# Kernel tuning notes

Hardware: AMD Instinct MI355X
Metric: run time of the kernel (lower is better)

## Reference

```python
import jax, jax.numpy as jnp
import numpy as np

EMB = 512
HEADS = 8
WINDOW = 128


def setup_inputs() -> dict:
    key = jax.random.key(0)
    ks = jax.random.split(key, 9)
    s = 1.0 / np.sqrt(EMB)
    x = jax.random.normal(ks[0], (2, 4096, EMB), dtype=jnp.float32)
    mk = lambda k: jax.random.uniform(k, (EMB, EMB), jnp.float32, -s, s)
    mb = lambda k: jax.random.uniform(k, (EMB,), jnp.float32, -s, s)
    return {
        "x": x,
        "Wq": mk(ks[1]), "bq": mb(ks[2]),
        "Wk": mk(ks[3]), "bk": mb(ks[4]),
        "Wv": mk(ks[5]), "bv": mb(ks[6]),
        "Wo": mk(ks[7]), "bo": mb(ks[8]),
    }


def _split_heads(y, b, n):
    # [b, n, emb] -> [b, h, n, d]
    return y.reshape(b, n, HEADS, EMB // HEADS).transpose(0, 2, 1, 3)


def reference(x, Wq, bq, Wk, bk, Wv, bv, Wo, bo):
    b, n, _ = x.shape
    q = _split_heads(x @ Wq.T + bq, b, n)
    k = _split_heads(x @ Wk.T + bk, b, n)
    v = _split_heads(x @ Wv.T + bv, b, n)
    energy = jnp.einsum('bhqd,bhkd->bhqk', q, k)  # [b,h,n,n]
    idx = jnp.arange(n)
    # banded mask: disallowed where |i - j| > window (matches torch loop)
    disallow = jnp.abs(idx[:, None] - idx[None, :]) > WINDOW
    fmin = jnp.float32(np.finfo(np.float32).min)
    energy = jnp.where(disallow[None, None], fmin, energy)
    att = jax.nn.softmax(energy / jnp.float32(np.sqrt(EMB)), axis=-1)
    out = jnp.einsum('bhql,bhld->bhqd', att, v)
    out = out.transpose(0, 2, 1, 3).reshape(b, n, EMB)
    return out @ Wo.T + bo
```

## Files before the change

### kernel.cpp

```cpp
#include <hip/hip_runtime.h>

#define EMB 512
#define HEADS 8
#define HD 64
#define NSEQ 4096
#define BATCH 2
#define WINDOW 128

typedef unsigned short u16;
typedef __attribute__((ext_vector_type(8))) short bf16x8;
typedef __attribute__((ext_vector_type(4))) float f32x4;

__device__ __forceinline__ float bf2f(u16 u) {
    union { unsigned int i; float f; } x;
    x.i = ((unsigned int)u) << 16;
    return x.f;
}

__device__ __forceinline__ u16 f2bf(float f) {
    union { float f; unsigned int i; } x;
    x.f = f;
    unsigned int i = x.i;
    unsigned int lsb = (i >> 16) & 1u;
    i += 0x7fffu + lsb;
    return (u16)(i >> 16);
}

__device__ __forceinline__ uint4 load8(const void* base, size_t off, int isbf) {
    if (isbf) {
        return *(const uint4*)((const u16*)base + off);
    } else {
        const float* f = (const float*)base + off;
        float4 a = *(const float4*)f;
        float4 b = *(const float4*)(f + 4);
        uint4 r;
        r.x = (unsigned)f2bf(a.x) | ((unsigned)f2bf(a.y) << 16);
        r.y = (unsigned)f2bf(a.z) | ((unsigned)f2bf(a.w) << 16);
        r.z = (unsigned)f2bf(b.x) | ((unsigned)f2bf(b.y) << 16);
        r.w = (unsigned)f2bf(b.z) | ((unsigned)f2bf(b.w) << 16);
        return r;
    }
}

__device__ __forceinline__ float loadScalar(const void* base, int i, int isbf) {
    return isbf ? bf2f(((const u16*)base)[i]) : ((const float*)base)[i];
}

__global__ void probe_dtypes(const void* p0, const void* p1, const void* p2,
                             const void* p3, const void* p4, const void* p5,
                             const void* p6, const void* p7, const void* p8,
                             int* flags)
{
    const void* ptrs[9] = {p0, p1, p2, p3, p4, p5, p6, p7, p8};
    const int lane = threadIdx.x;
    for (int i = 0; i < 9; ++i) {
        u16 w = ((const u16*)ptrs[i])[lane * 2];
        int e = (w >> 7) & 0xff;
        bool sane = (w == 0) || (e >= 100 && e <= 140);
        unsigned long long m = __ballot(sane);
        if (lane == 0) flags[i] = (__popcll(m) >= 48) ? 1 : 0;
    }
}

__global__ __launch_bounds__(256)
void qkv_gemm(const void* __restrict__ X,
              const void* __restrict__ Wq, const void* __restrict__ bq,
              const void* __restrict__ Wk, const void* __restrict__ bk,
              const void* __restrict__ Wv, const void* __restrict__ bv,
              u16* __restrict__ qo, u16* __restrict__ ko, u16* __restrict__ vo,
              const int* __restrict__ flags)
{
    __shared__ __align__(16) u16 As[128 * 32];
    __shared__ __align__(16) u16 Bs[128 * 32];

    const int tid  = threadIdx.x;
    const int wave = tid >> 6;
    const int lane = tid & 63;
    const int quad = lane >> 4;
    const int l16  = lane & 15;
    const int wm = wave >> 1, wn = wave & 1;

    const int m0 = blockIdx.x * 128;
    const int by = blockIdx.y;
    const int wsel = by >> 2;
    const int n0 = (by & 3) * 128;

    const void* W  = (wsel == 0) ? Wq : (wsel == 1) ? Wk : Wv;
    const void* bi = (wsel == 0) ? bq : (wsel == 1) ? bk : bv;
    u16* out       = (wsel == 0) ? qo : (wsel == 1) ? ko : vo;
    const float oscale = (wsel == 0) ? 0.04419417382415922f : 1.0f;

    const int fx = flags[0];
    const int fw = (wsel == 0) ? flags[1] : (wsel == 1) ? flags[3] : flags[5];
    const int fb = (wsel == 0) ? flags[2] : (wsel == 1) ? flags[4] : flags[6];

    f32x4 acc[4][4];
#pragma unroll
    for (int i = 0; i < 4; ++i)
#pragma unroll
        for (int j = 0; j < 4; ++j)
            acc[i][j] = (f32x4){0.f, 0.f, 0.f, 0.f};

    const int c1 = tid, c2 = tid + 256;
    const int r1 = c1 >> 2, k1 = (c1 & 3) * 8;
    const int r2 = c2 >> 2, k2 = (c2 & 3) * 8;

    for (int kt = 0; kt < 16; ++kt) {
        const int kk0 = kt * 32;
        uint4 a1 = load8(X, (size_t)(m0 + r1) * EMB + kk0 + k1, fx);
        uint4 a2 = load8(X, (size_t)(m0 + r2) * EMB + kk0 + k2, fx);
        uint4 b1 = load8(W, (size_t)(n0 + r1) * EMB + kk0 + k1, fw);
        uint4 b2 = load8(W, (size_t)(n0 + r2) * EMB + kk0 + k2, fw);
        __syncthreads();
        *(uint4*)&As[c1 * 8] = a1;
        *(uint4*)&As[c2 * 8] = a2;
        *(uint4*)&Bs[c1 * 8] = b1;
        *(uint4*)&Bs[c2 * 8] = b2;
        __syncthreads();

        bf16x8 af[4], bfr[4];
#pragma unroll
        for (int i = 0; i < 4; ++i)
            af[i] = *(const bf16x8*)&As[(wm * 64 + i * 16 + l16) * 32 + quad * 8];
#pragma unroll
        for (int j = 0; j < 4; ++j)
            bfr[j] = *(const bf16x8*)&Bs[(wn * 64 + j * 16 + l16) * 32 + quad * 8];
#pragma unroll
        for (int i = 0; i < 4; ++i)
#pragma unroll
            for (int j = 0; j < 4; ++j)
                acc[i][j] = __builtin_amdgcn_mfma_f32_16x16x32_bf16(af[i], bfr[j], acc[i][j], 0, 0, 0);
    }

#pragma unroll
    for (int j = 0; j < 4; ++j) {
        const int col = n0 + wn * 64 + j * 16 + l16;
        const float bv_ = loadScalar(bi, col, fb);
        const int h = col >> 6, d = col & 63;
#pragma unroll
        for (int i = 0; i < 4; ++i) {
#pragma unroll
            for (int r = 0; r < 4; ++r) {
                const int row = m0 + wm * 64 + i * 16 + quad * 4 + r;
                const int b = row >> 12, n = row & 4095;
                out[(((size_t)(b * HEADS + h) * NSEQ) + n) * HD + d] =
                    f2bf((acc[i][j][r] + bv_) * oscale);
            }
        }
    }
}

#define KP 72
__global__ __launch_bounds__(256)
void attn_mfma(const u16* __restrict__ q, const u16* __restrict__ k,
               const u16* __restrict__ v, u16* __restrict__ ao)
{
    __shared__ __align__(16) u16 Ks[64 * KP];
    __shared__ __align__(16) u16 Vt[64 * KP];
    __shared__ __align__(16) u16 Pb[4][16 * KP];

    const int tid  = threadIdx.x;
    const int wave = tid >> 6;
    const int lane = tid & 63;
    const int quad = lane >> 4;
    const int l16  = lane & 15;

    const int bh = blockIdx.y;
    const int q0 = blockIdx.x * 64;
    const int qw = q0 + wave * 16;
    const size_t base = (size_t)bh * NSEQ * HD;

    bf16x8 qa0 = *(const bf16x8*)(q + base + (size_t)(qw + l16) * HD + quad * 8);
    bf16x8 qa1 = *(const bf16x8*)(q + base + (size_t)(qw + l16) * HD + 32 + quad * 8);

    f32x4 O[4];
    float m_run[4], l_run[4];
#pragma unroll
    for (int t = 0; t < 4; ++t) O[t] = (f32x4){0.f, 0.f, 0.f, 0.f};
#pragma unroll
    for (int r = 0; r < 4; ++r) { m_run[r] = -1e30f; l_run[r] = 0.f; }

    for (int c = 0; c < 5; ++c) {
        const int kbase = q0 - 128 + c * 64;

        __syncthreads();
#pragma unroll
        for (int s = 0; s < 2; ++s) {
            const int idx = tid + s * 256;
            const int key = idx >> 3;
            const int d0  = (idx & 7) * 8;
            int kg = kbase + key;
            kg = (kg < 0) ? 0 : (kg > NSEQ - 1 ? NSEQ - 1 : kg);
            const size_t goff = base + (size_t)kg * HD + d0;
            uint4 kv = *(const uint4*)(k + goff);
            *(uint4*)&Ks[key * KP + d0] = kv;
            uint4 vv = *(const uint4*)(v + goff);
            u16 e[8];
            e[0] = (u16)(vv.x & 0xffff); e[1] = (u16)(vv.x >> 16);
            e[2] = (u16)(vv.y & 0xffff); e[3] = (u16)(vv.y >> 16);
            e[4] = (u16)(vv.z & 0xffff); e[5] = (u16)(vv.z >> 16);
            e[6] = (u16)(vv.w & 0xffff); e[7] = (u16)(vv.w >> 16);
#pragma unroll
            for (int j = 0; j < 8; ++j)
                Vt[(d0 + j) * KP + key] = e[j];
        }
        __syncthreads();

        f32x4 sv[4];
#pragma unroll
        for (int t = 0; t < 4; ++t) {
            bf16x8 b0 = *(const bf16x8*)&Ks[(t * 16 + l16) * KP + quad * 8];
            bf16x8 b1 = *(const bf16x8*)&Ks[(t * 16 + l16) * KP + 32 + quad * 8];
            f32x4 sacc = (f32x4){0.f, 0.f, 0.f, 0.f};
            sacc = __builtin_amdgcn_mfma_f32_16x16x32_bf16(qa0, b0, sacc, 0, 0, 0);
            sacc = __builtin_amdgcn_mfma_f32_16x16x32_bf16(qa1, b1, sacc, 0, 0, 0);
            sv[t] = sacc;
        }

#pragma unroll
        for (int t = 0; t < 4; ++t) {
            const int jg = kbase + t * 16 + l16;
            const bool jok = ((unsigned)jg) < (unsigned)NSEQ;
#pragma unroll
            for (int r = 0; r < 4; ++r) {
                const int iq = qw + quad * 4 + r;
                const bool band = ((unsigned)(iq - jg + WINDOW)) <= (unsigned)(2 * WINDOW);
                if (!(jok && band)) sv[t][r] = -1e30f;
            }
        }

        float mnew[4];
#pragma unroll
        for (int r = 0; r < 4; ++r)
            mnew[r] = fmaxf(fmaxf(sv[0][r], sv[1][r]), fmaxf(sv[2][r], sv[3][r]));
#pragma unroll
        for (int off = 1; off < 16; off <<= 1)
#pragma unroll
            for (int r = 0; r < 4; ++r)
                mnew[r] = fmaxf(mnew[r], __shfl_xor(mnew[r], off, 64));

        float alpha[4], mi[4];
#pragma unroll
        for (int r = 0; r < 4; ++r) {
            mi[r] = fmaxf(m_run[r], mnew[r]);
            alpha[r] = __expf(m_run[r] - mi[r]);
            m_run[r] = mi[r];
        }

        float p[4][4], lnew[4] = {0.f, 0.f, 0.f, 0.f};
#pragma unroll
        for (int t = 0; t < 4; ++t)
#pragma unroll
            for (int r = 0; r < 4; ++r) {
                float pv = (sv[t][r] > -1e29f) ? __expf(sv[t][r] - mi[r]) : 0.f;
                p[t][r] = pv;
                lnew[r] += pv;
            }
#pragma unroll
        for (int off = 1; off < 16; off <<= 1)
#pragma unroll
            for (int r = 0; r < 4; ++r)
                lnew[r] += __shfl_xor(lnew[r], off, 64);
#pragma unroll
        for (int r = 0; r < 4; ++r)
            l_run[r] = l_run[r] * alpha[r] + lnew[r];

#pragma unroll
        for (int t = 0; t < 4; ++t)
#pragma unroll
            for (int r = 0; r < 4; ++r)
                O[t][r] *= alpha[r];

#pragma unroll
        for (int t = 0; t < 4; ++t)
#pragma unroll
            for (int r = 0; r < 4; ++r)
                Pb[wave][(quad * 4 + r) * KP + t * 16 + l16] = f2bf(p[t][r]);

#pragma unroll
        for (int ks = 0; ks < 2; ++ks) {
            bf16x8 pa = *(const bf16x8*)&Pb[wave][l16 * KP + ks * 32 + quad * 8];
#pragma unroll
            for (int t = 0; t < 4; ++t) {
                bf16x8 vb = *(const bf16x8*)&Vt[(t * 16 + l16) * KP + ks * 32 + quad * 8];
                O[t] = __builtin_amdgcn_mfma_f32_16x16x32_bf16(pa, vb, O[t], 0, 0, 0);
            }
        }
    }

    const int bb = bh >> 3, hh = bh & 7;
    float rl[4];
#pragma unroll
    for (int r = 0; r < 4; ++r) rl[r] = 1.f / l_run[r];
#pragma unroll
    for (int t = 0; t < 4; ++t)
#pragma unroll
        for (int r = 0; r < 4; ++r) {
            const int iq = qw + quad * 4 + r;
            ao[((size_t)(bb * NSEQ + iq)) * EMB + hh * HD + t * 16 + l16] =
                f2bf(O[t][r] * rl[r]);
        }
}

__global__ __launch_bounds__(256)
void out_gemm(const u16* __restrict__ A, const void* __restrict__ W,
              const void* __restrict__ bias, void* __restrict__ out,
              const int* __restrict__ flags)
{
    __shared__ __align__(16) u16 As[128 * 32];
    __shared__ __align__(16) u16 Bs[128 * 32];

    const int tid  = threadIdx.x;
    const int wave = tid >> 6;
    const int lane = tid & 63;
    const int quad = lane >> 4;
    const int l16  = lane & 15;
    const int wm = wave >> 1, wn = wave & 1;

    const int m0 = blockIdx.x * 128;
    const int n0 = blockIdx.y * 128;

    const int fw = flags[7];
    const int fb = flags[8];
    const int fo = flags[0];

    f32x4 acc[4][4];
#pragma unroll
    for (int i = 0; i < 4; ++i)
#pragma unroll
        for (int j = 0; j < 4; ++j)
            acc[i][j] = (f32x4){0.f, 0.f, 0.f, 0.f};

    const int c1 = tid, c2 = tid + 256;
    const int r1 = c1 >> 2, k1 = (c1 & 3) * 8;
    const int r2 = c2 >> 2, k2 = (c2 & 3) * 8;

    for (int kt = 0; kt < 16; ++kt) {
        const int kk0 = kt * 32;
        uint4 a1 = *(const uint4*)(A + (size_t)(m0 + r1) * EMB + kk0 + k1);
        uint4 a2 = *(const uint4*)(A + (size_t)(m0 + r2) * EMB + kk0 + k2);
        uint4 b1 = load8(W, (size_t)(n0 + r1) * EMB + kk0 + k1, fw);
        uint4 b2 = load8(W, (size_t)(n0 + r2) * EMB + kk0 + k2, fw);
        __syncthreads();
        *(uint4*)&As[c1 * 8] = a1;
        *(uint4*)&As[c2 * 8] = a2;
        *(uint4*)&Bs[c1 * 8] = b1;
        *(uint4*)&Bs[c2 * 8] = b2;
        __syncthreads();

        bf16x8 af[4], bfr[4];
#pragma unroll
        for (int i = 0; i < 4; ++i)
            af[i] = *(const bf16x8*)&As[(wm * 64 + i * 16 + l16) * 32 + quad * 8];
#pragma unroll
        for (int j = 0; j < 4; ++j)
            bfr[j] = *(const bf16x8*)&Bs[(wn * 64 + j * 16 + l16) * 32 + quad * 8];
#pragma unroll
        for (int i = 0; i < 4; ++i)
#pragma unroll
            for (int j = 0; j < 4; ++j)
                acc[i][j] = __builtin_amdgcn_mfma_f32_16x16x32_bf16(af[i], bfr[j], acc[i][j], 0, 0, 0);
    }

#pragma unroll
    for (int j = 0; j < 4; ++j) {
        const int col = n0 + wn * 64 + j * 16 + l16;
        const float bv_ = loadScalar(bias, col, fb);
#pragma unroll
        for (int i = 0; i < 4; ++i) {
#pragma unroll
            for (int r = 0; r < 4; ++r) {
                const int row = m0 + wm * 64 + i * 16 + quad * 4 + r;
                const float val = acc[i][j][r] + bv_;
                const size_t idx = (size_t)row * EMB + col;
                if (fo) ((u16*)out)[idx] = f2bf(val);
                else    ((float*)out)[idx] = val;
            }
        }
    }
}

extern "C" void kernel_launch(void* const* d_in, const int* in_sizes, int n_in,
                              void* d_out, int out_size, void* d_ws, size_t ws_size,
                              hipStream_t stream)
{
    const size_t HSZ  = (size_t)BATCH * HEADS * NSEQ * HD;
    const size_t HSZB = HSZ * 2;
    char* base = (char*)d_ws;
    int* flags = (int*)base;
    const size_t off = 256;

    u16 *q, *k, *v, *ao;
    if (ws_size >= off + 4 * HSZB) {
        q  = (u16*)(base + off);
        k  = q + HSZ;
        v  = k + HSZ;
        ao = v + HSZ;
    } else if (ws_size >= off + 3 * HSZB) {
        q  = (u16*)d_out;
        k  = (u16*)(base + off);
        v  = k + HSZ;
        ao = v + HSZ;
    } else {
        q  = (u16*)d_out;
        k  = (u16*)(base + off);
        v  = k + HSZ;
        ao = (u16*)d_in[0];
    }

    probe_dtypes<<<1, 64, 0, stream>>>(d_in[0], d_in[1], d_in[2], d_in[3], d_in[4],
                                       d_in[5], d_in[6], d_in[7], d_in[8], flags);
    qkv_gemm<<<dim3(64, 12), 256, 0, stream>>>(d_in[0], d_in[1], d_in[2], d_in[3],
                                               d_in[4], d_in[5], d_in[6], q, k, v, flags);
    attn_mfma<<<dim3(64, 16), 256, 0, stream>>>(q, k, v, ao);
    out_gemm<<<dim3(64, 4), 256, 0, stream>>>(ao, d_in[7], d_in[8], d_out, flags);
}
```

Baseline: 177.8 us.

## Prefetch next tiles into registers, pad GEMM LDS rows, inline dtype probe

Both GEMMs and the attention kernel now load the next K tile (and the next K/V chunk) into registers while the current tile is being consumed, so global load latency overlaps with MFMA work. GEMM shared-memory rows are padded from 32 to 40 elements to reduce LDS bank conflicts on fragment reads. The separate dtype-probe kernel launch is removed, and each block runs the probe inline with a wave ballot, with one thread still writing flags[0] for out_gemm. The cost is higher register pressure from holding prefetched raw fp32 data, plus redundant probe loads in every block.

```diff
diff --git a/kernel.cpp b/kernel.cpp
--- a/kernel.cpp
+++ b/kernel.cpp
@@ -10,6 +10,8 @@
 typedef unsigned short u16;
 typedef __attribute__((ext_vector_type(8))) short bf16x8;
 typedef __attribute__((ext_vector_type(4))) float f32x4;
+
+#define GP 40
 
 __device__ __forceinline__ float bf2f(u16 u) {
     union { unsigned int i; float f; } x;
@@ -26,40 +28,43 @@
     return (u16)(i >> 16);
 }
 
-__device__ __forceinline__ uint4 load8(const void* base, size_t off, int isbf) {
+struct raw8 { uint4 lo, hi; };
+
+__device__ __forceinline__ raw8 loadraw8(const void* base, size_t off, int isbf) {
+    raw8 r;
     if (isbf) {
-        return *(const uint4*)((const u16*)base + off);
+        r.lo = *(const uint4*)((const u16*)base + off);
     } else {
         const float* f = (const float*)base + off;
-        float4 a = *(const float4*)f;
-        float4 b = *(const float4*)(f + 4);
-        uint4 r;
-        r.x = (unsigned)f2bf(a.x) | ((unsigned)f2bf(a.y) << 16);
-        r.y = (unsigned)f2bf(a.z) | ((unsigned)f2bf(a.w) << 16);
-        r.z = (unsigned)f2bf(b.x) | ((unsigned)f2bf(b.y) << 16);
-        r.w = (unsigned)f2bf(b.z) | ((unsigned)f2bf(b.w) << 16);
-        return r;
-    }
+        r.lo = *(const uint4*)f;
+        r.hi = *(const uint4*)(f + 4);
+    }
+    return r;
+}
+
+__device__ __forceinline__ uint4 cvt8(const raw8& r, int isbf) {
+    if (isbf) return r.lo;
+    const float* a = (const float*)&r.lo;
+    const float* b = (const float*)&r.hi;
+    uint4 o;
+    o.x = (unsigned)f2bf(a[0]) | ((unsigned)f2bf(a[1]) << 16);
+    o.y = (unsigned)f2bf(a[2]) | ((unsigned)f2bf(a[3]) << 16);
+    o.z = (unsigned)f2bf(b[0]) | ((unsigned)f2bf(b[1]) << 16);
+    o.w = (unsigned)f2bf(b[2]) | ((unsigned)f2bf(b[3]) << 16);
+    return o;
 }
 
 __device__ __forceinline__ float loadScalar(const void* base, int i, int isbf) {
     return isbf ? bf2f(((const u16*)base)[i]) : ((const float*)base)[i];
 }
 
-__global__ void probe_dtypes(const void* p0, const void* p1, const void* p2,
-                             const void* p3, const void* p4, const void* p5,
-                             const void* p6, const void* p7, const void* p8,
-                             int* flags)
-{
-    const void* ptrs[9] = {p0, p1, p2, p3, p4, p5, p6, p7, p8};
-    const int lane = threadIdx.x;
-    for (int i = 0; i < 9; ++i) {
-        u16 w = ((const u16*)ptrs[i])[lane * 2];
-        int e = (w >> 7) & 0xff;
-        bool sane = (w == 0) || (e >= 100 && e <= 140);
-        unsigned long long m = __ballot(sane);
-        if (lane == 0) flags[i] = (__popcll(m) >= 48) ? 1 : 0;
-    }
+__device__ __forceinline__ int probe_bf16(const void* p) {
+    const int lane = threadIdx.x & 63;
+    u16 w = ((const u16*)p)[lane * 2];
+    int e = (w >> 7) & 0xff;
+    bool sane = (w == 0) || (e >= 100 && e <= 140);
+    unsigned long long m = __ballot(sane);
+    return __popcll(m) >= 48;
 }
 
 __global__ __launch_bounds__(256)
@@ -68,10 +73,10 @@
               const void* __restrict__ Wk, const void* __restrict__ bk,
               const void* __restrict__ Wv, const void* __restrict__ bv,
               u16* __restrict__ qo, u16* __restrict__ ko, u16* __restrict__ vo,
-              const int* __restrict__ flags)
+              int* __restrict__ flags)
 {
-    __shared__ __align__(16) u16 As[128 * 32];
-    __shared__ __align__(16) u16 Bs[128 * 32];
+    __shared__ __align__(16) u16 As[128 * GP];
+    __shared__ __align__(16) u16 Bs[128 * GP];
 
     const int tid  = threadIdx.x;
     const int wave = tid >> 6;
@@ -90,9 +95,10 @@
     u16* out       = (wsel == 0) ? qo : (wsel == 1) ? ko : vo;
     const float oscale = (wsel == 0) ? 0.04419417382415922f : 1.0f;
 
-    const int fx = flags[0];
-    const int fw = (wsel == 0) ? flags[1] : (wsel == 1) ? flags[3] : flags[5];
-    const int fb = (wsel == 0) ? flags[2] : (wsel == 1) ? flags[4] : flags[6];
+    const int fx = probe_bf16(X);
+    const int fw = probe_bf16(W);
+    const int fb = probe_bf16(bi);
+    if (blockIdx.x == 0 && by == 0 && tid == 0) flags[0] = fx;
 
     f32x4 acc[4][4];
 #pragma unroll
@@ -105,26 +111,34 @@
     const int r1 = c1 >> 2, k1 = (c1 & 3) * 8;
     const int r2 = c2 >> 2, k2 = (c2 & 3) * 8;
 
+    raw8 a1 = loadraw8(X, (size_t)(m0 + r1) * EMB + k1, fx);
+    raw8 a2 = loadraw8(X, (size_t)(m0 + r2) * EMB + k2, fx);
+    raw8 b1 = loadraw8(W, (size_t)(n0 + r1) * EMB + k1, fw);
+    raw8 b2 = loadraw8(W, (size_t)(n0 + r2) * EMB + k2, fw);
+
     for (int kt = 0; kt < 16; ++kt) {
-        const int kk0 = kt * 32;
-        uint4 a1 = load8(X, (size_t)(m0 + r1) * EMB + kk0 + k1, fx);
-        uint4 a2 = load8(X, (size_t)(m0 + r2) * EMB + kk0 + k2, fx);
-        uint4 b1 = load8(W, (size_t)(n0 + r1) * EMB + kk0 + k1, fw);
-        uint4 b2 = load8(W, (size_t)(n0 + r2) * EMB + kk0 + k2, fw);
-        __syncthreads();
-        *(uint4*)&As[c1 * 8] = a1;
-        *(uint4*)&As[c2 * 8] = a2;
-        *(uint4*)&Bs[c1 * 8] = b1;
-        *(uint4*)&Bs[c2 * 8] = b2;
-        __syncthreads();
+        __syncthreads();
+        *(uint4*)&As[r1 * GP + k1] = cvt8(a1, fx);
+        *(uint4*)&As[r2 * GP + k2] = cvt8(a2, fx);
+        *(uint4*)&Bs[r1 * GP + k1] = cvt8(b1, fw);
+        *(uint4*)&Bs[r2 * GP + k2] = cvt8(b2, fw);
+        __syncthreads();
+
+        if (kt < 15) {
+            const int kk0 = (kt + 1) * 32;
+            a1 = loadraw8(X, (size_t)(m0 + r1) * EMB + kk0 + k1, fx);
+            a2 = loadraw8(X, (size_t)(m0 + r2) * EMB + kk0 + k2, fx);
+            b1 = loadraw8(W, (size_t)(n0 + r1) * EMB + kk0 + k1, fw);
+            b2 = loadraw8(W, (size_t)(n0 + r2) * EMB + kk0 + k2, fw);
+        }
 
         bf16x8 af[4], bfr[4];
 #pragma unroll
         for (int i = 0; i < 4; ++i)
-            af[i] = *(const bf16x8*)&As[(wm * 64 + i * 16 + l16) * 32 + quad * 8];
+            af[i] = *(const bf16x8*)&As[(wm * 64 + i * 16 + l16) * GP + quad * 8];
 #pragma unroll
         for (int j = 0; j < 4; ++j)
-            bfr[j] = *(const bf16x8*)&Bs[(wn * 64 + j * 16 + l16) * 32 + quad * 8];
+            bfr[j] = *(const bf16x8*)&Bs[(wn * 64 + j * 16 + l16) * GP + quad * 8];
 #pragma unroll
         for (int i = 0; i < 4; ++i)
 #pragma unroll
@@ -180,21 +194,28 @@
 #pragma unroll
     for (int r = 0; r < 4; ++r) { m_run[r] = -1e30f; l_run[r] = 0.f; }
 
+    const int key_s[2] = { (tid) >> 3, (tid + 256) >> 3 };
+    const int d0_s[2]  = { (tid & 7) * 8, (tid & 7) * 8 };
+
+    uint4 pkv[2], pvv[2];
+#pragma unroll
+    for (int s = 0; s < 2; ++s) {
+        int kg = q0 - 128 + key_s[s];
+        kg = (kg < 0) ? 0 : (kg > NSEQ - 1 ? NSEQ - 1 : kg);
+        const size_t goff = base + (size_t)kg * HD + d0_s[s];
+        pkv[s] = *(const uint4*)(k + goff);
+        pvv[s] = *(const uint4*)(v + goff);
+    }
+
     for (int c = 0; c < 5; ++c) {
         const int kbase = q0 - 128 + c * 64;
 
         __syncthreads();
 #pragma unroll
         for (int s = 0; s < 2; ++s) {
-            const int idx = tid + s * 256;
-            const int key = idx >> 3;
-            const int d0  = (idx & 7) * 8;
-            int kg = kbase + key;
-            kg = (kg < 0) ? 0 : (kg > NSEQ - 1 ? NSEQ - 1 : kg);
-            const size_t goff = base + (size_t)kg * HD + d0;
-            uint4 kv = *(const uint4*)(k + goff);
-            *(uint4*)&Ks[key * KP + d0] = kv;
-            uint4 vv = *(const uint4*)(v + goff);
+            const int key = key_s[s], d0 = d0_s[s];
+            *(uint4*)&Ks[key * KP + d0] = pkv[s];
+            uint4 vv = pvv[s];
             u16 e[8];
             e[0] = (u16)(vv.x & 0xffff); e[1] = (u16)(vv.x >> 16);
             e[2] = (u16)(vv.y & 0xffff); e[3] = (u16)(vv.y >> 16);
@@ -205,6 +226,17 @@
                 Vt[(d0 + j) * KP + key] = e[j];
         }
         __syncthreads();
+
+        if (c < 4) {
+#pragma unroll
+            for (int s = 0; s < 2; ++s) {
+                int kg = kbase + 64 + key_s[s];
+                kg = (kg < 0) ? 0 : (kg > NSEQ - 1 ? NSEQ - 1 : kg);
+                const size_t goff = base + (size_t)kg * HD + d0_s[s];
+                pkv[s] = *(const uint4*)(k + goff);
+                pvv[s] = *(const uint4*)(v + goff);
+            }
+        }
 
         f32x4 sv[4];
 #pragma unroll
@@ -307,8 +339,8 @@
               const void* __restrict__ bias, void* __restrict__ out,
               const int* __restrict__ flags)
 {
-    __shared__ __align__(16) u16 As[128 * 32];
-    __shared__ __align__(16) u16 Bs[128 * 32];
+    __shared__ __align__(16) u16 As[128 * GP];
+    __shared__ __align__(16) u16 Bs[128 * GP];
 
     const int tid  = threadIdx.x;
     const int wave = tid >> 6;
@@ -320,8 +352,8 @@
     const int m0 = blockIdx.x * 128;
     const int n0 = blockIdx.y * 128;
 
-    const int fw = flags[7];
-    const int fb = flags[8];
+    const int fw = probe_bf16(W);
+    const int fb = probe_bf16(bias);
     const int fo = flags[0];
 
     f32x4 acc[4][4];
@@ -335,26 +367,34 @@
     const int r1 = c1 >> 2, k1 = (c1 & 3) * 8;
     const int r2 = c2 >> 2, k2 = (c2 & 3) * 8;
 
+    raw8 a1 = loadraw8(A, (size_t)(m0 + r1) * EMB + k1, 1);
+    raw8 a2 = loadraw8(A, (size_t)(m0 + r2) * EMB + k2, 1);
+    raw8 b1 = loadraw8(W, (size_t)(n0 + r1) * EMB + k1, fw);
+    raw8 b2 = loadraw8(W, (size_t)(n0 + r2) * EMB + k2, fw);
+
     for (int kt = 0; kt < 16; ++kt) {
-        const int kk0 = kt * 32;
-        uint4 a1 = *(const uint4*)(A + (size_t)(m0 + r1) * EMB + kk0 + k1);
-        uint4 a2 = *(const uint4*)(A + (size_t)(m0 + r2) * EMB + kk0 + k2);
-        uint4 b1 = load8(W, (size_t)(n0 + r1) * EMB + kk0 + k1, fw);
-        uint4 b2 = load8(W, (size_t)(n0 + r2) * EMB + kk0 + k2, fw);
-        __syncthreads();
-        *(uint4*)&As[c1 * 8] = a1;
-        *(uint4*)&As[c2 * 8] = a2;
-        *(uint4*)&Bs[c1 * 8] = b1;
-        *(uint4*)&Bs[c2 * 8] = b2;
-        __syncthreads();
+        __syncthreads();
+        *(uint4*)&As[r1 * GP + k1] = a1.lo;
+        *(uint4*)&As[r2 * GP + k2] = a2.lo;
+        *(uint4*)&Bs[r1 * GP + k1] = cvt8(b1, fw);
+        *(uint4*)&Bs[r2 * GP + k2] = cvt8(b2, fw);
+        __syncthreads();
+
+        if (kt < 15) {
+            const int kk0 = (kt + 1) * 32;
+            a1 = loadraw8(A, (size_t)(m0 + r1) * EMB + kk0 + k1, 1);
+            a2 = loadraw8(A, (size_t)(m0 + r2) * EMB + kk0 + k2, 1);
+            b1 = loadraw8(W, (size_t)(n0 + r1) * EMB + kk0 + k1, fw);
+            b2 = loadraw8(W, (size_t)(n0 + r2) * EMB + kk0 + k2, fw);
+        }
 
         bf16x8 af[4], bfr[4];
 #pragma unroll
         for (int i = 0; i < 4; ++i)
-            af[i] = *(const bf16x8*)&As[(wm * 64 + i * 16 + l16) * 32 + quad * 8];
+            af[i] = *(const bf16x8*)&As[(wm * 64 + i * 16 + l16) * GP + quad * 8];
 #pragma unroll
         for (int j = 0; j < 4; ++j)
-            bfr[j] = *(const bf16x8*)&Bs[(wn * 64 + j * 16 + l16) * 32 + quad * 8];
+            bfr[j] = *(const bf16x8*)&Bs[(wn * 64 + j * 16 + l16) * GP + quad * 8];
 #pragma unroll
         for (int i = 0; i < 4; ++i)
 #pragma unroll
@@ -408,8 +448,6 @@
         ao = (u16*)d_in[0];
     }
 
-    probe_dtypes<<<1, 64, 0, stream>>>(d_in[0], d_in[1], d_in[2], d_in[3], d_in[4],
-                                       d_in[5], d_in[6], d_in[7], d_in[8], flags);
     qkv_gemm<<<dim3(64, 12), 256, 0, stream>>>(d_in[0], d_in[1], d_in[2], d_in[3],
                                                d_in[4], d_in[5], d_in[6], q, k, v, flags);
     attn_mfma<<<dim3(64, 16), 256, 0, stream>>>(q, k, v, ao);
```

Result: faster. 168.8 us (-5.0%).
